# Kernel tuning notes

Hardware: AMD Instinct MI355X
Metric: run time of the kernel (lower is better)

The kernel has to match this reference:

```python
import jax, jax.numpy as jnp
import numpy as np

N_ENT = 100000
D1 = 200
DA = 30
DS = 30
DO = 20
NUM_SYM = 3
NUM_ASYM = 5
N_REL = 11
BATCH = 1024
REL_PERM = np.array([8, 0, 3, 9, 4, 5, 6, 7, 1, 10, 2], dtype=np.int64)


def build_indices(d1):
    # Replicates the torch index construction exactly (numpy, trace-time constants).
    symu = np.stack([
        np.concatenate([np.zeros(i, np.int64),
                        np.arange((2 * d1 - i + 1) * i // 2, (2 * d1 - i) * (i + 1) // 2, dtype=np.int64)])
        for i in range(d1)])
    syml = np.stack([
        np.concatenate([np.zeros(i + 1, np.int64),
                        np.arange((2 * d1 - i + 1) * i // 2 + 1, (2 * d1 - i) * (i + 1) // 2, dtype=np.int64)])
        for i in range(d1)]).T
    sym_index = symu + syml  # (d1, d1) indices into W1 columns (symmetric layout)
    asym_index = np.stack([
        np.concatenate([np.zeros(i + 1, np.int64),
                        np.arange((2 * d1 - i - 1) * i // 2 + 1, (2 * d1 - i - 2) * (i + 1) // 2 + 1, dtype=np.int64)])
        for i in range(d1)])  # (d1, d1) indices into [0|W2] columns (strict upper layout)
    return sym_index, asym_index


def _batchnorm(x, gamma, beta, eps=1e-5):
    # BatchNorm1d in training mode: biased batch statistics over the batch dim.
    m = jnp.mean(x, axis=0)
    v = jnp.var(x, axis=0)
    return (x - m) * jax.lax.rsqrt(v + eps) * gamma + beta


def setup_inputs() -> dict:
    key = jax.random.key(0)
    ks = jax.random.split(key, 10)
    return {
        "E": 0.1 * jax.random.normal(ks[0], (N_ENT, D1), jnp.float32),
        "R1": 0.1 * jax.random.normal(ks[1], (NUM_SYM, DA), jnp.float32),
        "R2": 0.1 * jax.random.normal(ks[2], (NUM_ASYM, DS), jnp.float32),
        "R3": 0.1 * jax.random.normal(ks[3], (N_REL - NUM_SYM - NUM_ASYM, DA + DS + DO), jnp.float32),
        "W1": jax.random.uniform(ks[4], (DS, D1 * (D1 + 1) // 2), jnp.float32, -1.0, 1.0),
        "W2": jax.random.uniform(ks[5], (DA, D1 * (D1 - 1) // 2), jnp.float32, -1.0, 1.0),
        "W3": jax.random.uniform(ks[6], (DO, D1, D1), jnp.float32, -1.0, 1.0),
        "bn0_gamma": jnp.ones((D1,), jnp.float32),
        "bn0_beta": jnp.zeros((D1,), jnp.float32),
        "bn1_gamma": jnp.ones((D1,), jnp.float32),
        "bn1_beta": jnp.zeros((D1,), jnp.float32),
        "e1_idx": jax.random.randint(ks[7], (BATCH,), 0, N_ENT),
        "r_idx": jax.random.randint(ks[8], (BATCH,), 0, N_REL),
    }


def reference(E, R1, R2, R3, W1, W2, W3, bn0_gamma, bn0_beta, bn1_gamma, bn1_beta, e1_idx, r_idx):
    d1 = E.shape[1]
    sym_index, asym_index = build_indices(d1)

    # construct_RW: relation matrix R (N_REL, ds+da+do) with zero-padded blocks
    R = jnp.concatenate([
        jnp.concatenate([R1, jnp.zeros((NUM_SYM, DA + DO), R1.dtype)], axis=1),
        jnp.concatenate([jnp.zeros((NUM_ASYM, DS), R2.dtype), R2,
                         jnp.zeros((NUM_ASYM, DO), R2.dtype)], axis=1),
        R3,
    ], axis=0)

    # core tensor W (ds+da+do, d1, d1): symmetric slices, antisymmetric slices, free slices
    W2_temp = jnp.concatenate([jnp.zeros((DA, 1), W2.dtype), W2], axis=1)[:, asym_index]
    W = jnp.concatenate([
        W1[:, sym_index],
        W2_temp - jnp.swapaxes(W2_temp, 1, 2),
        W3,
    ], axis=0)

    r = R[jnp.asarray(REL_PERM)[r_idx]]             # (b, K)
    W_mat = jnp.einsum('ijk,bi->bjk', W, r)          # (b, d1, d1)  large intermediate
    x = _batchnorm(E[e1_idx], bn0_gamma, bn0_beta)   # (b, d1)
    x = jnp.einsum('bjk,bj->bk', W_mat, x)           # (b, d1)
    x = _batchnorm(x, bn1_gamma, bn1_beta)
    scores = jnp.einsum('bk,nk->bn', x, E)           # (b, n_ent)
    return jax.nn.sigmoid(scores)
```

## Files before the change

kernel.cpp:

```cpp
#include <hip/hip_runtime.h>
#include <stdint.h>

#define N_ENT 100000
#define D1    200
#define BATCH 1024
#define KPAD  224
#define NPAD  100096
#define NTILES 782

typedef unsigned short ushort_t;
typedef __attribute__((ext_vector_type(8))) short short8;
typedef __attribute__((ext_vector_type(4))) float f32x4;

__constant__ int c_perm[11] = {8, 0, 3, 9, 4, 5, 6, 7, 1, 10, 2};

__device__ __forceinline__ unsigned short f2bf(float f) {
    unsigned int u = __float_as_uint(f);
    unsigned int r = (u + 0x7fffu + ((u >> 16) & 1u)) >> 16;
    return (unsigned short)r;
}

__device__ __forceinline__ int sym_idx(int a, int b) {
    int i = a < b ? a : b;
    int j = a < b ? b : a;
    return i * D1 - (i * (i - 1)) / 2 + (j - i);
}
__device__ __forceinline__ int asym_idx(int i, int j) {
    return i * D1 - (i * (i + 1)) / 2 + (j - i - 1);
}

__global__ void conv_E(const float* __restrict__ E, ushort_t* __restrict__ Epad) {
    int idx = blockIdx.x * 256 + threadIdx.x;
    if (idx >= NPAD * KPAD) return;
    int n = idx / KPAD;
    int k = idx - n * KPAD;
    float v = 0.f;
    if (n < N_ENT && k < D1) v = E[n * D1 + k];
    Epad[idx] = f2bf(v);
}

__global__ void build_M(const float* __restrict__ R1, const float* __restrict__ R2,
                        const float* __restrict__ R3, const float* __restrict__ W1,
                        const float* __restrict__ W2, const float* __restrict__ W3,
                        float* __restrict__ M) {
    int rel = blockIdx.y;
    int e = blockIdx.x * 256 + threadIdx.x;
    if (e >= D1 * D1) return;
    int j = e / D1;
    int k = e - j * D1;
    float acc = 0.f;
    if (rel < 3) {
        int si = sym_idx(j, k);
        #pragma unroll 6
        for (int i = 0; i < 30; i++) acc += R1[rel * 30 + i] * W1[i * 20100 + si];
    } else if (rel < 8) {
        if (j != k) {
            int ai = (j < k) ? asym_idx(j, k) : asym_idx(k, j);
            float s = (j < k) ? 1.f : -1.f;
            #pragma unroll 6
            for (int i = 0; i < 30; i++) acc += R2[(rel - 3) * 30 + i] * s * W2[i * 19900 + ai];
        }
    } else {
        const float* r3 = R3 + (rel - 8) * 80;
        int si = sym_idx(j, k);
        #pragma unroll 6
        for (int i = 0; i < 30; i++) acc += r3[i] * W1[i * 20100 + si];
        if (j != k) {
            int ai = (j < k) ? asym_idx(j, k) : asym_idx(k, j);
            float s = (j < k) ? 1.f : -1.f;
            #pragma unroll 6
            for (int i = 0; i < 30; i++) acc += r3[30 + i] * s * W2[i * 19900 + ai];
        }
        #pragma unroll 5
        for (int i = 0; i < 20; i++) acc += r3[60 + i] * W3[i * 40000 + e];
    }
    M[rel * 40000 + e] = acc;
}

__global__ void bn0_stats(const float* __restrict__ E, const int* __restrict__ e1_idx,
                          const float* __restrict__ gamma, const float* __restrict__ beta,
                          float* __restrict__ scale, float* __restrict__ shift) {
    int f = blockIdx.x;
    int tid = threadIdx.x;
    float s = 0.f, sq = 0.f;
    for (int b = tid; b < BATCH; b += 256) {
        float v = E[e1_idx[b] * D1 + f];
        s += v; sq += v * v;
    }
    __shared__ float ls[256], lq[256];
    ls[tid] = s; lq[tid] = sq;
    __syncthreads();
    for (int off = 128; off > 0; off >>= 1) {
        if (tid < off) { ls[tid] += ls[tid + off]; lq[tid] += lq[tid + off]; }
        __syncthreads();
    }
    if (tid == 0) {
        float m = ls[0] * (1.f / BATCH);
        float var = lq[0] * (1.f / BATCH) - m * m;
        float rstd = rsqrtf(var + 1e-5f);
        scale[f] = rstd * gamma[f];
        shift[f] = beta[f] - m * rstd * gamma[f];
    }
}

__global__ void bn1_stats(const float* __restrict__ y,
                          const float* __restrict__ gamma, const float* __restrict__ beta,
                          float* __restrict__ scale, float* __restrict__ shift) {
    int f = blockIdx.x;
    int tid = threadIdx.x;
    float s = 0.f, sq = 0.f;
    for (int b = tid; b < BATCH; b += 256) {
        float v = y[b * D1 + f];
        s += v; sq += v * v;
    }
    __shared__ float ls[256], lq[256];
    ls[tid] = s; lq[tid] = sq;
    __syncthreads();
    for (int off = 128; off > 0; off >>= 1) {
        if (tid < off) { ls[tid] += ls[tid + off]; lq[tid] += lq[tid + off]; }
        __syncthreads();
    }
    if (tid == 0) {
        float m = ls[0] * (1.f / BATCH);
        float var = lq[0] * (1.f / BATCH) - m * m;
        float rstd = rsqrtf(var + 1e-5f);
        scale[f] = rstd * gamma[f];
        shift[f] = beta[f] - m * rstd * gamma[f];
    }
}

__global__ void xw_kernel(const float* __restrict__ E, const int* __restrict__ e1_idx,
                          const int* __restrict__ r_idx,
                          const float* __restrict__ scale0, const float* __restrict__ shift0,
                          const float* __restrict__ M, float* __restrict__ y) {
    int b = blockIdx.x;
    int tid = threadIdx.x;
    __shared__ float xs[D1];
    __shared__ int s_rel;
    if (tid == 0) s_rel = c_perm[r_idx[b]];
    int e1 = e1_idx[b];
    if (tid < D1) xs[tid] = E[e1 * D1 + tid] * scale0[tid] + shift0[tid];
    __syncthreads();
    if (tid < D1) {
        const float* Mr = M + s_rel * 40000;
        float acc = 0.f;
        #pragma unroll 8
        for (int j = 0; j < D1; j++) acc += xs[j] * Mr[j * D1 + tid];
        y[b * D1 + tid] = acc;
    }
}

__global__ void x2pad_kernel(const float* __restrict__ y,
                             const float* __restrict__ scale1, const float* __restrict__ shift1,
                             ushort_t* __restrict__ x2) {
    int idx = blockIdx.x * 256 + threadIdx.x;
    if (idx >= BATCH * KPAD) return;
    int b = idx / KPAD;
    int k = idx - b * KPAD;
    float v = 0.f;
    if (k < D1) v = y[b * D1 + k] * scale1[k] + shift1[k];
    x2[idx] = f2bf(v);
}

__device__ __forceinline__ void gld_lds16(const void* g, void* l) {
    __builtin_amdgcn_global_load_lds(
        (const __attribute__((address_space(1))) unsigned int*)(uintptr_t)g,
        (__attribute__((address_space(3))) unsigned int*)(unsigned int)(uintptr_t)l,
        16, 0, 0);
}

__global__ __launch_bounds__(256) void gemm_score(const ushort_t* __restrict__ x2,
                                                  const ushort_t* __restrict__ Epad,
                                                  float* __restrict__ out) {
    __shared__ ushort_t As[128 * 32];
    __shared__ ushort_t Bs[128 * 32];
    const int tid = threadIdx.x;
    const int wave = tid >> 6;
    const int lane = tid & 63;
    const int wm = wave >> 1, wn = wave & 1;
    const int quad = lane >> 4, l16 = lane & 15;
    const int tile_n = blockIdx.x * 128;
    const int tile_m = blockIdx.y * 128;

    const int srow = tid >> 2;
    const int sseg = tid & 3;

    f32x4 acc[4][4];
    #pragma unroll
    for (int i = 0; i < 4; i++)
        #pragma unroll
        for (int j = 0; j < 4; j++) acc[i][j] = (f32x4){0.f, 0.f, 0.f, 0.f};

    for (int kb = 0; kb < KPAD; kb += 32) {
        #pragma unroll
        for (int rr = 0; rr < 2; rr++) {
            const ushort_t* ga = x2 + (tile_m + rr * 64 + srow) * KPAD + kb + sseg * 8;
            gld_lds16(ga, &As[rr * 2048 + wave * 512]);
            const ushort_t* gb = Epad + (tile_n + rr * 64 + srow) * KPAD + kb + sseg * 8;
            gld_lds16(gb, &Bs[rr * 2048 + wave * 512]);
        }
        __syncthreads();

        short8 a_frag[4], b_frag[4];
        #pragma unroll
        for (int f = 0; f < 4; f++) {
            a_frag[f] = *(const short8*)&As[(wm * 64 + f * 16 + l16) * 32 + quad * 8];
            b_frag[f] = *(const short8*)&Bs[(wn * 64 + f * 16 + l16) * 32 + quad * 8];
        }
        #pragma unroll
        for (int fm = 0; fm < 4; fm++)
            #pragma unroll
            for (int fn = 0; fn < 4; fn++)
                acc[fm][fn] = __builtin_amdgcn_mfma_f32_16x16x32_bf16(
                    a_frag[fm], b_frag[fn], acc[fm][fn], 0, 0, 0);
        __syncthreads();
    }

    #pragma unroll
    for (int fm = 0; fm < 4; fm++) {
        int m = tile_m + wm * 64 + fm * 16 + quad * 4;
        #pragma unroll
        for (int fn = 0; fn < 4; fn++) {
            int n = tile_n + wn * 64 + fn * 16 + l16;
            if (n < N_ENT) {
                float* po = out + (size_t)m * N_ENT + n;
                #pragma unroll
                for (int r = 0; r < 4; r++) {
                    float v = acc[fm][fn][r];
                    po[(size_t)r * N_ENT] = 1.f / (1.f + __expf(-v));
                }
            }
        }
    }
}

extern "C" void kernel_launch(void* const* d_in, const int* in_sizes, int n_in,
                              void* d_out, int out_size, void* d_ws, size_t ws_size,
                              hipStream_t stream) {
    const float* E  = (const float*)d_in[0];
    const float* R1 = (const float*)d_in[1];
    const float* R2 = (const float*)d_in[2];
    const float* R3 = (const float*)d_in[3];
    const float* W1 = (const float*)d_in[4];
    const float* W2 = (const float*)d_in[5];
    const float* W3 = (const float*)d_in[6];
    const float* g0 = (const float*)d_in[7];
    const float* b0 = (const float*)d_in[8];
    const float* g1 = (const float*)d_in[9];
    const float* b1 = (const float*)d_in[10];
    const int* e1_idx = (const int*)d_in[11];
    const int* r_idx  = (const int*)d_in[12];
    float* out = (float*)d_out;

    char* ws = (char*)d_ws;
    ushort_t* Epad = (ushort_t*)ws;
    float* M       = (float*)(ws + 44843008);
    float* scale0  = (float*)(ws + 46603008);
    float* shift0  = scale0 + D1;
    float* scale1  = shift0 + D1;
    float* shift1  = scale1 + D1;
    float* y       = shift1 + D1;
    ushort_t* x2   = (ushort_t*)(y + BATCH * D1);

    conv_E<<<(NPAD * KPAD + 255) / 256, 256, 0, stream>>>(E, Epad);
    build_M<<<dim3((D1 * D1 + 255) / 256, 11), 256, 0, stream>>>(R1, R2, R3, W1, W2, W3, M);
    bn0_stats<<<D1, 256, 0, stream>>>(E, e1_idx, g0, b0, scale0, shift0);
    xw_kernel<<<BATCH, 256, 0, stream>>>(E, e1_idx, r_idx, scale0, shift0, M, y);
    bn1_stats<<<D1, 256, 0, stream>>>(y, g1, b1, scale1, shift1);
    x2pad_kernel<<<(BATCH * KPAD + 255) / 256, 256, 0, stream>>>(y, scale1, shift1, x2);
    gemm_score<<<dim3(NTILES, BATCH / 128), 256, 0, stream>>>(x2, Epad, out);
}
```

Before: 635.7 us.

## Fuse bf16 conversion and BN1 affine into score GEMM tile loads

Drops the separate kernels that padded and converted E and the normalized activations to bf16. The score GEMM now reads fp32 y and E directly, applies the BN1 scale and shift, and converts to bf16 while staging into shared memory. It also writes the sigmoid output with nontemporal stores. This removes a large intermediate write and read plus two launches. In exchange, the asynchronous global-to-LDS loads become synchronous register loads, and each E tile is read in fp32 by every M block, which doubles the bytes fetched per tile.

```diff
diff --git a/kernel.cpp b/kernel.cpp
--- a/kernel.cpp
+++ b/kernel.cpp
@@ -5,7 +5,6 @@
 #define D1    200
 #define BATCH 1024
 #define KPAD  224
-#define NPAD  100096
 #define NTILES 782
 
 typedef unsigned short ushort_t;
@@ -27,16 +26,6 @@
 }
 __device__ __forceinline__ int asym_idx(int i, int j) {
     return i * D1 - (i * (i + 1)) / 2 + (j - i - 1);
-}
-
-__global__ void conv_E(const float* __restrict__ E, ushort_t* __restrict__ Epad) {
-    int idx = blockIdx.x * 256 + threadIdx.x;
-    if (idx >= NPAD * KPAD) return;
-    int n = idx / KPAD;
-    int k = idx - n * KPAD;
-    float v = 0.f;
-    if (n < N_ENT && k < D1) v = E[n * D1 + k];
-    Epad[idx] = f2bf(v);
 }
 
 __global__ void build_M(const float* __restrict__ R1, const float* __restrict__ R2,
@@ -150,30 +139,14 @@
     }
 }
 
-__global__ void x2pad_kernel(const float* __restrict__ y,
-                             const float* __restrict__ scale1, const float* __restrict__ shift1,
-                             ushort_t* __restrict__ x2) {
-    int idx = blockIdx.x * 256 + threadIdx.x;
-    if (idx >= BATCH * KPAD) return;
-    int b = idx / KPAD;
-    int k = idx - b * KPAD;
-    float v = 0.f;
-    if (k < D1) v = y[b * D1 + k] * scale1[k] + shift1[k];
-    x2[idx] = f2bf(v);
-}
-
-__device__ __forceinline__ void gld_lds16(const void* g, void* l) {
-    __builtin_amdgcn_global_load_lds(
-        (const __attribute__((address_space(1))) unsigned int*)(uintptr_t)g,
-        (__attribute__((address_space(3))) unsigned int*)(unsigned int)(uintptr_t)l,
-        16, 0, 0);
-}
-
-__global__ __launch_bounds__(256) void gemm_score(const ushort_t* __restrict__ x2,
-                                                  const ushort_t* __restrict__ Epad,
+__global__ __launch_bounds__(256) void gemm_score(const float* __restrict__ y,
+                                                  const float* __restrict__ E,
+                                                  const float* __restrict__ scale1,
+                                                  const float* __restrict__ shift1,
                                                   float* __restrict__ out) {
     __shared__ ushort_t As[128 * 32];
     __shared__ ushort_t Bs[128 * 32];
+    __shared__ float s_sc[KPAD], s_sh[KPAD];
     const int tid = threadIdx.x;
     const int wave = tid >> 6;
     const int lane = tid & 63;
@@ -185,6 +158,12 @@
     const int srow = tid >> 2;
     const int sseg = tid & 3;
 
+    if (tid < KPAD) {
+        s_sc[tid] = (tid < D1) ? scale1[tid] : 0.f;
+        s_sh[tid] = (tid < D1) ? shift1[tid] : 0.f;
+    }
+    __syncthreads();
+
     f32x4 acc[4][4];
     #pragma unroll
     for (int i = 0; i < 4; i++)
@@ -192,12 +171,35 @@
         for (int j = 0; j < 4; j++) acc[i][j] = (f32x4){0.f, 0.f, 0.f, 0.f};
 
     for (int kb = 0; kb < KPAD; kb += 32) {
+        const int k0 = kb + sseg * 8;
+        const bool kin = (k0 < D1);
         #pragma unroll
         for (int rr = 0; rr < 2; rr++) {
-            const ushort_t* ga = x2 + (tile_m + rr * 64 + srow) * KPAD + kb + sseg * 8;
-            gld_lds16(ga, &As[rr * 2048 + wave * 512]);
-            const ushort_t* gb = Epad + (tile_n + rr * 64 + srow) * KPAD + kb + sseg * 8;
-            gld_lds16(gb, &Bs[rr * 2048 + wave * 512]);
+            const int row = rr * 64 + srow;
+            short8 ha;
+            if (kin) {
+                const float* p = y + (tile_m + row) * D1 + k0;
+                #pragma unroll
+                for (int j = 0; j < 8; j++) {
+                    float x = p[j] * s_sc[k0 + j] + s_sh[k0 + j];
+                    ha[j] = (short)f2bf(x);
+                }
+            } else {
+                #pragma unroll
+                for (int j = 0; j < 8; j++) ha[j] = 0;
+            }
+            *(short8*)&As[row * 32 + sseg * 8] = ha;
+            const int gn = tile_n + row;
+            short8 hb;
+            if (kin && gn < N_ENT) {
+                const float* q = E + (size_t)gn * D1 + k0;
+                #pragma unroll
+                for (int j = 0; j < 8; j++) hb[j] = (short)f2bf(q[j]);
+            } else {
+                #pragma unroll
+                for (int j = 0; j < 8; j++) hb[j] = 0;
+            }
+            *(short8*)&Bs[row * 32 + sseg * 8] = hb;
         }
         __syncthreads();
 
@@ -227,7 +229,8 @@
                 #pragma unroll
                 for (int r = 0; r < 4; r++) {
                     float v = acc[fm][fn][r];
-                    po[(size_t)r * N_ENT] = 1.f / (1.f + __expf(-v));
+                    float sg = 1.f / (1.f + __expf(-v));
+                    __builtin_nontemporal_store(sg, po + (size_t)r * N_ENT);
                 }
             }
         }
@@ -253,20 +256,16 @@
     float* out = (float*)d_out;
 
     char* ws = (char*)d_ws;
-    ushort_t* Epad = (ushort_t*)ws;
-    float* M       = (float*)(ws + 44843008);
-    float* scale0  = (float*)(ws + 46603008);
-    float* shift0  = scale0 + D1;
-    float* scale1  = shift0 + D1;
-    float* shift1  = scale1 + D1;
-    float* y       = shift1 + D1;
-    ushort_t* x2   = (ushort_t*)(y + BATCH * D1);
-
-    conv_E<<<(NPAD * KPAD + 255) / 256, 256, 0, stream>>>(E, Epad);
+    float* M      = (float*)ws;
+    float* scale0 = (float*)(ws + 1760000);
+    float* shift0 = scale0 + D1;
+    float* scale1 = shift0 + D1;
+    float* shift1 = scale1 + D1;
+    float* y      = shift1 + D1;
+
+    bn0_stats<<<D1, 256, 0, stream>>>(E, e1_idx, g0, b0, scale0, shift0);
     build_M<<<dim3((D1 * D1 + 255) / 256, 11), 256, 0, stream>>>(R1, R2, R3, W1, W2, W3, M);
-    bn0_stats<<<D1, 256, 0, stream>>>(E, e1_idx, g0, b0, scale0, shift0);
     xw_kernel<<<BATCH, 256, 0, stream>>>(E, e1_idx, r_idx, scale0, shift0, M, y);
     bn1_stats<<<D1, 256, 0, stream>>>(y, g1, b1, scale1, shift1);
-    x2pad_kernel<<<(BATCH * KPAD + 255) / 256, 256, 0, stream>>>(y, scale1, shift1, x2);
-    gemm_score<<<dim3(NTILES, BATCH / 128), 256, 0, stream>>>(x2, Epad, out);
-}
+    gemm_score<<<dim3(NTILES, BATCH / 128), 256, 0, stream>>>(y, E, scale1, shift1, out);
+}
```

Result: slower. 674.6 us (+6.1%).
